# Kernel optimization log

Measured on AMD Instinct MI355X. Metric: run time of the kernel, lower is better.

Reference implementation:

```python
import jax, jax.numpy as jnp
import numpy as np

IN_ = 64
FEATURE = 1024
BATCH = 256

def setup_inputs() -> dict:
    key = jax.random.key(0)
    kx, kw = jax.random.split(key)
    x = jax.random.normal(kx, (BATCH, IN_, FEATURE), dtype=jnp.float32)
    # W[i] corresponds to torch Linear weight of shape [out_features, in_features]
    # scaled like torch's default kaiming-uniform-ish init (bound = 1/sqrt(fan_in))
    bound = 1.0 / np.sqrt(FEATURE)
    W = jax.random.uniform(kw, (IN_, FEATURE, FEATURE), dtype=jnp.float32,
                           minval=-bound, maxval=bound)
    return {"x": x, "W": W}

def reference(x, W):
    # Per-position independent linear: out[b,i,o] = sum_f x[b,i,f] * W[i,o,f]
    # (torch Linear computes x @ W^T). Single batched GEMM via einsum.
    return jnp.einsum('bif,iof->bio', x, W)
```

## Files before the change

### kernel.cpp

```cpp
#include <hip/hip_runtime.h>
#include <hip/hip_bf16.h>

#define IN_CNT 64
#define FEAT   1024
#define BATCH  256

#define BM 256
#define BN 256
#define BK 32
#define KT (FEAT / BK)

typedef __attribute__((ext_vector_type(4))) float f32x4;
typedef __attribute__((ext_vector_type(8))) short short8;

__device__ __forceinline__ short f2bf(float f) {
    __hip_bfloat16 h = __float2bfloat16(f);
    return __builtin_bit_cast(short, h);
}

__device__ __forceinline__ short8 pack8(f32x4 a, f32x4 b) {
    short8 v;
    v[0] = f2bf(a[0]); v[1] = f2bf(a[1]); v[2] = f2bf(a[2]); v[3] = f2bf(a[3]);
    v[4] = f2bf(b[0]); v[5] = f2bf(b[1]); v[6] = f2bf(b[2]); v[7] = f2bf(b[3]);
    return v;
}

__device__ __forceinline__ void barrier_nodrain() {
    asm volatile("s_waitcnt lgkmcnt(0)" ::: "memory");
    __builtin_amdgcn_s_barrier();
    asm volatile("" ::: "memory");
}

__device__ __forceinline__ int SWZ(int r) { return (r + (r >> 2)) & 3; }

__global__ __launch_bounds__(512, 2)
void split_linear_kernel(const float* __restrict__ x,
                         const float* __restrict__ W,
                         float* __restrict__ out)
{
    __shared__ __align__(16) short lds[2 * 2 * BM * BK];

    const int tid = threadIdx.x;

    const int bid = blockIdx.x;
    const int swz = ((bid & 7) << 5) | (bid >> 3);
    const int gi   = swz >> 2;
    const int ncol = (swz & 3) << 8;

    const int r   = tid >> 1;
    const int h   = tid & 1;
    const int swr = SWZ(r);
    const int sl0 = ((2 * h) ^ swr) << 3;
    const int sl1 = ((2 * h + 1) ^ swr) << 3;

    const float* Abase = x + ((size_t)r * IN_CNT + gi) * FEAT + h * 16;
    const float* Bbase = W + ((size_t)gi * FEAT + ncol + r) * FEAT + h * 16;

    const int lane = tid & 63;
    const int wid  = tid >> 6;
    const int wm   = wid >> 2;
    const int wn   = wid & 3;
    const int lr   = lane & 15;
    const int lh   = lane >> 4;
    const int slr  = (lh ^ SWZ(lr)) << 3;

    f32x4 sA[2][4], sB[2][4];
    f32x4 acc[8][4];
#pragma unroll
    for (int m = 0; m < 8; ++m)
#pragma unroll
        for (int n = 0; n < 4; ++n)
            acc[m][n] = (f32x4){0.f, 0.f, 0.f, 0.f};

    auto LOADT = [&](int kt, int s) {
        const float* qa = Abase + kt * BK;
        const float* qb = Bbase + kt * BK;
#pragma unroll
        for (int i = 0; i < 4; ++i) {
            sA[s][i] = *(const f32x4*)(qa + i * 4);
            sB[s][i] = *(const f32x4*)(qb + i * 4);
        }
    };

    auto WRITET = [&](int s, int b) {
        short* dst = lds + b * 16384 + r * 32;
        *(short8*)(dst + sl0)        = pack8(sA[s][0], sA[s][1]);
        *(short8*)(dst + sl1)        = pack8(sA[s][2], sA[s][3]);
        *(short8*)(dst + 8192 + sl0) = pack8(sB[s][0], sB[s][1]);
        *(short8*)(dst + 8192 + sl1) = pack8(sB[s][2], sB[s][3]);
    };

    auto COMPUTE = [&](int b) {
        const short* base = lds + b * 16384;
        short8 bf[4];
#pragma unroll
        for (int nf = 0; nf < 4; ++nf)
            bf[nf] = *(const short8*)(base + 8192 + (wn * 64 + nf * 16 + lr) * 32 + slr);
#pragma unroll
        for (int mf = 0; mf < 8; ++mf) {
            short8 af = *(const short8*)(base + (wm * 128 + mf * 16 + lr) * 32 + slr);
#pragma unroll
            for (int nf = 0; nf < 4; ++nf)
                acc[mf][nf] = __builtin_amdgcn_mfma_f32_16x16x32_bf16(
                    af, bf[nf], acc[mf][nf], 0, 0, 0);
        }
    };

    LOADT(0, 0);
    LOADT(1, 1);
    WRITET(0, 0);
    LOADT(2, 0);
    barrier_nodrain();

    for (int kt = 0; kt < KT; kt += 2) {
        WRITET(1, 1);
        if (kt + 3 < KT) LOADT(kt + 3, 1);
        COMPUTE(0);
        barrier_nodrain();
        if (kt + 2 < KT) WRITET(0, 0);
        if (kt + 4 < KT) LOADT(kt + 4, 0);
        COMPUTE(1);
        barrier_nodrain();
    }

    float* elds = (float*)lds;
#pragma unroll
    for (int s = 0; s < 4; ++s) {
        barrier_nodrain();
        if (wm == (s >> 1)) {
            const int mfb = (s & 1) * 4;
#pragma unroll
            for (int f = 0; f < 4; ++f)
#pragma unroll
                for (int nf = 0; nf < 4; ++nf)
#pragma unroll
                    for (int j = 0; j < 4; ++j)
                        elds[(f * 16 + lh * 4 + j) * 256 + wn * 64 + nf * 16 + lr]
                            = acc[mfb + f][nf][j];
        }
        barrier_nodrain();
#pragma unroll
        for (int rr = 0; rr < 8; ++rr) {
            const int rowl = wid * 8 + rr;
            f32x4 v = *(const f32x4*)&elds[rowl * 256 + lane * 4];
            const int m = s * 64 + rowl;
            *(f32x4*)&out[((size_t)m * IN_CNT + gi) * FEAT + ncol + lane * 4] = v;
        }
    }
}

extern "C" void kernel_launch(void* const* d_in, const int* in_sizes, int n_in,
                              void* d_out, int out_size, void* d_ws, size_t ws_size,
                              hipStream_t stream) {
    const float* x   = (const float*)d_in[0];
    const float* W   = (const float*)d_in[1];
    float*       out = (float*)d_out;

    dim3 grid(IN_CNT * (FEAT / BN));
    dim3 block(512);
    hipLaunchKernelGGL(split_linear_kernel, grid, block, 0, stream, x, W, out);
}
```

Baseline: 93.23 us.

## Double the K tile, coalesce global loads, XOR-swizzle LDS, pad epilogue stride

Raises BK from 32 to 64 and runs one LDS buffer per K step, halving the number of block barriers. Global loads are remapped so 16 consecutive lanes read one contiguous 256-byte row segment. A new XOR swizzle on the bf16 LDS tiles keeps the MFMA fragment reads free of bank conflicts. The epilogue staging row is padded to 260 floats to cut bank conflicts on the transposed writes. The tiles now use 128 KB of LDS, so only one block fits per CU.

```diff
diff --git a/kernel.cpp b/kernel.cpp
--- a/kernel.cpp
+++ b/kernel.cpp
@@ -7,21 +7,21 @@
 
 #define BM 256
 #define BN 256
-#define BK 32
+#define BK 64
 #define KT (FEAT / BK)
 
 typedef __attribute__((ext_vector_type(4))) float f32x4;
-typedef __attribute__((ext_vector_type(8))) short short8;
+typedef __attribute__((ext_vector_type(4))) short bf16x4;
+typedef __attribute__((ext_vector_type(8))) short bf16x8;
 
 __device__ __forceinline__ short f2bf(float f) {
     __hip_bfloat16 h = __float2bfloat16(f);
     return __builtin_bit_cast(short, h);
 }
 
-__device__ __forceinline__ short8 pack8(f32x4 a, f32x4 b) {
-    short8 v;
+__device__ __forceinline__ bf16x4 pack4(f32x4 a) {
+    bf16x4 v;
     v[0] = f2bf(a[0]); v[1] = f2bf(a[1]); v[2] = f2bf(a[2]); v[3] = f2bf(a[3]);
-    v[4] = f2bf(b[0]); v[5] = f2bf(b[1]); v[6] = f2bf(b[2]); v[7] = f2bf(b[3]);
     return v;
 }
 
@@ -31,14 +31,12 @@
     asm volatile("" ::: "memory");
 }
 
-__device__ __forceinline__ int SWZ(int r) { return (r + (r >> 2)) & 3; }
-
 __global__ __launch_bounds__(512, 2)
 void split_linear_kernel(const float* __restrict__ x,
                          const float* __restrict__ W,
                          float* __restrict__ out)
 {
-    __shared__ __align__(16) short lds[2 * 2 * BM * BK];
+    __shared__ __align__(16) short lds[65536];
 
     const int tid = threadIdx.x;
 
@@ -47,24 +45,19 @@
     const int gi   = swz >> 2;
     const int ncol = (swz & 3) << 8;
 
-    const int r   = tid >> 1;
-    const int h   = tid & 1;
-    const int swr = SWZ(r);
-    const int sl0 = ((2 * h) ^ swr) << 3;
-    const int sl1 = ((2 * h + 1) ^ swr) << 3;
-
-    const float* Abase = x + ((size_t)r * IN_CNT + gi) * FEAT + h * 16;
-    const float* Bbase = W + ((size_t)gi * FEAT + ncol + r) * FEAT + h * 16;
-
     const int lane = tid & 63;
     const int wid  = tid >> 6;
     const int wm   = wid >> 2;
     const int wn   = wid & 3;
     const int lr   = lane & 15;
     const int lh   = lane >> 4;
-    const int slr  = (lh ^ SWZ(lr)) << 3;
 
-    f32x4 sA[2][4], sB[2][4];
+    const int srow = wid * 4 + lh;
+    const int gpos = lr;
+    const float* Abase = x + ((size_t)srow * IN_CNT + gi) * FEAT + gpos * 4;
+    const float* Bbase = W + ((size_t)gi * FEAT + ncol + srow) * FEAT + gpos * 4;
+
+    f32x4 ra[8], rb[8];
     f32x4 acc[8][4];
 #pragma unroll
     for (int m = 0; m < 8; ++m)
@@ -72,57 +65,63 @@
         for (int n = 0; n < 4; ++n)
             acc[m][n] = (f32x4){0.f, 0.f, 0.f, 0.f};
 
-    auto LOADT = [&](int kt, int s) {
-        const float* qa = Abase + kt * BK;
-        const float* qb = Bbase + kt * BK;
+    auto LOADT = [&](int kt) {
 #pragma unroll
-        for (int i = 0; i < 4; ++i) {
-            sA[s][i] = *(const f32x4*)(qa + i * 4);
-            sB[s][i] = *(const f32x4*)(qb + i * 4);
+        for (int i = 0; i < 8; ++i) {
+            ra[i] = *(const f32x4*)(Abase + (size_t)kt * BK + (size_t)i * (32 * IN_CNT * FEAT));
+            rb[i] = *(const f32x4*)(Bbase + (size_t)kt * BK + (size_t)i * (32 * FEAT));
         }
     };
 
-    auto WRITET = [&](int s, int b) {
-        short* dst = lds + b * 16384 + r * 32;
-        *(short8*)(dst + sl0)        = pack8(sA[s][0], sA[s][1]);
-        *(short8*)(dst + sl1)        = pack8(sA[s][2], sA[s][3]);
-        *(short8*)(dst + 8192 + sl0) = pack8(sB[s][0], sB[s][1]);
-        *(short8*)(dst + 8192 + sl1) = pack8(sB[s][2], sB[s][3]);
+    auto WRITET = [&](int b) {
+        short* base = lds + b * 32768;
+#pragma unroll
+        for (int i = 0; i < 8; ++i) {
+            const int r  = srow + i * 32;
+            const int s8 = gpos ^ ((r & 7) << 1);
+            *(bf16x4*)&base[r * 64 + s8 * 4]         = pack4(ra[i]);
+            *(bf16x4*)&base[16384 + r * 64 + s8 * 4] = pack4(rb[i]);
+        }
     };
 
     auto COMPUTE = [&](int b) {
-        const short* base = lds + b * 16384;
-        short8 bf[4];
+        const short* baseA = lds + b * 32768;
+        const short* baseB = baseA + 16384;
 #pragma unroll
-        for (int nf = 0; nf < 4; ++nf)
-            bf[nf] = *(const short8*)(base + 8192 + (wn * 64 + nf * 16 + lr) * 32 + slr);
+        for (int ks = 0; ks < 2; ++ks) {
+            const int t = ks * 4 + lh;
+            bf16x8 bf[4];
 #pragma unroll
-        for (int mf = 0; mf < 8; ++mf) {
-            short8 af = *(const short8*)(base + (wm * 128 + mf * 16 + lr) * 32 + slr);
+            for (int nf = 0; nf < 4; ++nf) {
+                const int r = wn * 64 + nf * 16 + lr;
+                bf[nf] = *(const bf16x8*)&baseB[r * 64 + ((t ^ (r & 7)) << 3)];
+            }
 #pragma unroll
-            for (int nf = 0; nf < 4; ++nf)
-                acc[mf][nf] = __builtin_amdgcn_mfma_f32_16x16x32_bf16(
-                    af, bf[nf], acc[mf][nf], 0, 0, 0);
+            for (int mf = 0; mf < 8; ++mf) {
+                const int r = wm * 128 + mf * 16 + lr;
+                bf16x8 af = *(const bf16x8*)&baseA[r * 64 + ((t ^ (r & 7)) << 3)];
+#pragma unroll
+                for (int nf = 0; nf < 4; ++nf)
+                    acc[mf][nf] = __builtin_amdgcn_mfma_f32_16x16x32_bf16(
+                        af, bf[nf], acc[mf][nf], 0, 0, 0);
+            }
         }
     };
 
-    LOADT(0, 0);
-    LOADT(1, 1);
-    WRITET(0, 0);
-    LOADT(2, 0);
+    LOADT(0);
+    WRITET(0);
+    LOADT(1);
     barrier_nodrain();
 
-    for (int kt = 0; kt < KT; kt += 2) {
-        WRITET(1, 1);
-        if (kt + 3 < KT) LOADT(kt + 3, 1);
-        COMPUTE(0);
-        barrier_nodrain();
-        if (kt + 2 < KT) WRITET(0, 0);
-        if (kt + 4 < KT) LOADT(kt + 4, 0);
-        COMPUTE(1);
+    for (int kt = 0; kt < KT; ++kt) {
+        const int b = kt & 1;
+        if (kt + 1 < KT) WRITET(b ^ 1);
+        if (kt + 2 < KT) LOADT(kt + 2);
+        COMPUTE(b);
         barrier_nodrain();
     }
 
+#define ELD 260
     float* elds = (float*)lds;
 #pragma unroll
     for (int s = 0; s < 4; ++s) {
@@ -135,18 +134,19 @@
                 for (int nf = 0; nf < 4; ++nf)
 #pragma unroll
                     for (int j = 0; j < 4; ++j)
-                        elds[(f * 16 + lh * 4 + j) * 256 + wn * 64 + nf * 16 + lr]
+                        elds[(f * 16 + lh * 4 + j) * ELD + wn * 64 + nf * 16 + lr]
                             = acc[mfb + f][nf][j];
         }
         barrier_nodrain();
 #pragma unroll
         for (int rr = 0; rr < 8; ++rr) {
             const int rowl = wid * 8 + rr;
-            f32x4 v = *(const f32x4*)&elds[rowl * 256 + lane * 4];
+            f32x4 v = *(const f32x4*)&elds[rowl * ELD + lane * 4];
             const int m = s * 64 + rowl;
             *(f32x4*)&out[((size_t)m * IN_CNT + gi) * FEAT + ncol + lane * 4] = v;
         }
     }
+#undef ELD
 }
 
 extern "C" void kernel_launch(void* const* d_in, const int* in_sizes, int n_in,
```

Result: slower. 106.3 us (+14.0%).

## Coalesce global loads with 8 threads per row and reswizzle shared-memory tiles

Applied to the files above, without the earlier changes.

Global loads now map eight consecutive threads to one 128-byte row segment instead of two threads per row with 64-byte spans, which should improve coalescing. The LDS tile layout changes to pair rows into 64-element lines with an XOR swizzle, writing 4-element bf16 chunks instead of 8. The epilogue staging buffer is padded to a 260-float row stride to reduce bank conflicts. Narrower LDS stores double the store instruction count, and the enlarged buffer uses more shared memory, which may affect occupancy.

```diff
diff --git a/kernel.cpp b/kernel.cpp
--- a/kernel.cpp
+++ b/kernel.cpp
@@ -11,17 +11,17 @@
 #define KT (FEAT / BK)
 
 typedef __attribute__((ext_vector_type(4))) float f32x4;
-typedef __attribute__((ext_vector_type(8))) short short8;
+typedef __attribute__((ext_vector_type(4))) short bf16x4;
+typedef __attribute__((ext_vector_type(8))) short bf16x8;
 
 __device__ __forceinline__ short f2bf(float f) {
     __hip_bfloat16 h = __float2bfloat16(f);
     return __builtin_bit_cast(short, h);
 }
 
-__device__ __forceinline__ short8 pack8(f32x4 a, f32x4 b) {
-    short8 v;
+__device__ __forceinline__ bf16x4 pack4(f32x4 a) {
+    bf16x4 v;
     v[0] = f2bf(a[0]); v[1] = f2bf(a[1]); v[2] = f2bf(a[2]); v[3] = f2bf(a[3]);
-    v[4] = f2bf(b[0]); v[5] = f2bf(b[1]); v[6] = f2bf(b[2]); v[7] = f2bf(b[3]);
     return v;
 }
 
@@ -31,14 +31,12 @@
     asm volatile("" ::: "memory");
 }
 
-__device__ __forceinline__ int SWZ(int r) { return (r + (r >> 2)) & 3; }
-
 __global__ __launch_bounds__(512, 2)
 void split_linear_kernel(const float* __restrict__ x,
                          const float* __restrict__ W,
                          float* __restrict__ out)
 {
-    __shared__ __align__(16) short lds[2 * 2 * BM * BK];
+    __shared__ __align__(16) short lds[33280];
 
     const int tid = threadIdx.x;
 
@@ -47,22 +45,20 @@
     const int gi   = swz >> 2;
     const int ncol = (swz & 3) << 8;
 
-    const int r   = tid >> 1;
-    const int h   = tid & 1;
-    const int swr = SWZ(r);
-    const int sl0 = ((2 * h) ^ swr) << 3;
-    const int sl1 = ((2 * h + 1) ^ swr) << 3;
-
-    const float* Abase = x + ((size_t)r * IN_CNT + gi) * FEAT + h * 16;
-    const float* Bbase = W + ((size_t)gi * FEAT + ncol + r) * FEAT + h * 16;
-
     const int lane = tid & 63;
     const int wid  = tid >> 6;
     const int wm   = wid >> 2;
     const int wn   = wid & 3;
     const int lr   = lane & 15;
     const int lh   = lane >> 4;
-    const int slr  = (lh ^ SWZ(lr)) << 3;
+
+    const int srow = tid >> 3;
+    const int g    = tid & 7;
+    const int wsh = (((((srow & 1) << 2) + (g >> 1)) ^ ((srow >> 1) & 7)) << 3)
+                    + ((g & 1) << 2);
+
+    const float* Abase = x + ((size_t)srow * IN_CNT + gi) * FEAT + g * 4;
+    const float* Bbase = W + ((size_t)gi * FEAT + ncol + srow) * FEAT + g * 4;
 
     f32x4 sA[2][4], sB[2][4];
     f32x4 acc[8][4];
@@ -73,32 +69,38 @@
             acc[m][n] = (f32x4){0.f, 0.f, 0.f, 0.f};
 
     auto LOADT = [&](int kt, int s) {
-        const float* qa = Abase + kt * BK;
-        const float* qb = Bbase + kt * BK;
 #pragma unroll
-        for (int i = 0; i < 4; ++i) {
-            sA[s][i] = *(const f32x4*)(qa + i * 4);
-            sB[s][i] = *(const f32x4*)(qb + i * 4);
+        for (int p = 0; p < 4; ++p) {
+            sA[s][p] = *(const f32x4*)(Abase + (size_t)kt * BK + (size_t)p * (64 * IN_CNT * FEAT));
+            sB[s][p] = *(const f32x4*)(Bbase + (size_t)kt * BK + (size_t)p * (64 * FEAT));
         }
     };
 
     auto WRITET = [&](int s, int b) {
-        short* dst = lds + b * 16384 + r * 32;
-        *(short8*)(dst + sl0)        = pack8(sA[s][0], sA[s][1]);
-        *(short8*)(dst + sl1)        = pack8(sA[s][2], sA[s][3]);
-        *(short8*)(dst + 8192 + sl0) = pack8(sB[s][0], sB[s][1]);
-        *(short8*)(dst + 8192 + sl1) = pack8(sB[s][2], sB[s][3]);
+        short* base = lds + b * 16384;
+#pragma unroll
+        for (int p = 0; p < 4; ++p) {
+            const int sr = (srow >> 1) + p * 32;
+            *(bf16x4*)&base[sr * 64 + wsh]        = pack4(sA[s][p]);
+            *(bf16x4*)&base[8192 + sr * 64 + wsh] = pack4(sB[s][p]);
+        }
     };
 
+    const int rsh = ((((lr & 1) << 2) + lh) ^ ((lr >> 1) & 7)) << 3;
+
     auto COMPUTE = [&](int b) {
-        const short* base = lds + b * 16384;
-        short8 bf[4];
+        const short* baseA = lds + b * 16384;
+        const short* baseB = baseA + 8192;
+        bf16x8 bf[4];
 #pragma unroll
-        for (int nf = 0; nf < 4; ++nf)
-            bf[nf] = *(const short8*)(base + 8192 + (wn * 64 + nf * 16 + lr) * 32 + slr);
+        for (int nf = 0; nf < 4; ++nf) {
+            const int sr = wn * 32 + nf * 8 + (lr >> 1);
+            bf[nf] = *(const bf16x8*)&baseB[sr * 64 + rsh];
+        }
 #pragma unroll
         for (int mf = 0; mf < 8; ++mf) {
-            short8 af = *(const short8*)(base + (wm * 128 + mf * 16 + lr) * 32 + slr);
+            const int sr = wm * 64 + mf * 8 + (lr >> 1);
+            bf16x8 af = *(const bf16x8*)&baseA[sr * 64 + rsh];
 #pragma unroll
             for (int nf = 0; nf < 4; ++nf)
                 acc[mf][nf] = __builtin_amdgcn_mfma_f32_16x16x32_bf16(
@@ -123,6 +125,7 @@
         barrier_nodrain();
     }
 
+#define ELD 260
     float* elds = (float*)lds;
 #pragma unroll
     for (int s = 0; s < 4; ++s) {
@@ -135,18 +138,19 @@
                 for (int nf = 0; nf < 4; ++nf)
 #pragma unroll
                     for (int j = 0; j < 4; ++j)
-                        elds[(f * 16 + lh * 4 + j) * 256 + wn * 64 + nf * 16 + lr]
+                        elds[(f * 16 + lh * 4 + j) * ELD + wn * 64 + nf * 16 + lr]
                             = acc[mfb + f][nf][j];
         }
         barrier_nodrain();
 #pragma unroll
         for (int rr = 0; rr < 8; ++rr) {
             const int rowl = wid * 8 + rr;
-            f32x4 v = *(const f32x4*)&elds[rowl * 256 + lane * 4];
+            f32x4 v = *(const f32x4*)&elds[rowl * ELD + lane * 4];
             const int m = s * 64 + rowl;
             *(f32x4*)&out[((size_t)m * IN_CNT + gi) * FEAT + ncol + lane * 4] = v;
         }
     }
+#undef ELD
 }
 
 extern "C" void kernel_launch(void* const* d_in, const int* in_sizes, int n_in,
```

Result: slower. 105.2 us (+12.9%).
